# Kernel tuning notes

Hardware: AMD Instinct MI355X
Metric: run time of the kernel (lower is better)

The kernel has to match this reference:

```python
import jax, jax.numpy as jnp
import numpy as np

MIN_K = 1024  # hard-negative mining floor per image (per_image=True branch)


def setup_inputs() -> dict:
    key = jax.random.key(0)
    k1, k2 = jax.random.split(key)
    B, C, D, H, W = 4, 3, 64, 256, 256
    inp = jax.random.normal(k1, (B, C, D, H, W), dtype=jnp.float32)
    tgt = jax.random.randint(k2, (B, D, H, W), 0, C, dtype=jnp.int64)
    return {"input": inp, "target": tgt}


def reference(input, target):
    b = input.shape[0]
    # per-pixel cross-entropy: -log_softmax over class dim, gathered at target
    logp = jax.nn.log_softmax(input, axis=1)                      # [B,C,D,H,W]
    ce = -jnp.take_along_axis(logp, target[:, None].astype(jnp.int32), axis=1)[:, 0]
    loss = ce.reshape(b, -1)                                      # [B, N]
    tflat = target.reshape(b, -1)                                 # [B, N]
    N = loss.shape[1]

    fg = tflat > 0                                                # [B, N]
    fg_num = fg.sum(axis=1)                                       # [B] int
    bg_num = N - fg_num                                           # [B] int
    k = jnp.minimum(bg_num, jnp.maximum(fg_num, MIN_K))           # [B] int

    # foreground term: mean of fg losses (0 if no fg)
    fg_sum = jnp.where(fg, loss, 0.0).sum(axis=1)                 # [B]
    fg_term = jnp.where(fg_num > 0,
                        fg_sum / jnp.maximum(fg_num, 1).astype(loss.dtype), 0.0)

    # background term: mean of top-k hardest bg losses (data-dependent k, fixed shapes)
    bg_masked = jnp.where(fg, -jnp.inf, loss)                     # fg -> -inf, never selected
    sorted_desc = -jnp.sort(-bg_masked, axis=1)                   # [B, N] descending
    sel = jnp.arange(N)[None, :] < k[:, None]                     # first k entries
    bg_sum = jnp.where(sel, sorted_desc, 0.0).sum(axis=1)         # [B]
    bg_term = jnp.where(bg_num > 0,
                        bg_sum / jnp.maximum(k, 1).astype(loss.dtype), 0.0)

    return jnp.sum(fg_term + bg_term) / b
```

## Files before the change

### kernel.cpp

```cpp
#include <hip/hip_runtime.h>

#define NPIX 4194304
#define BATCH 4
#define MINK 1024ULL
#define NBINS 4096
#define G1 1024
#define HG 256

typedef unsigned long long u64;
typedef int vint4 __attribute__((ext_vector_type(4)));

__device__ __forceinline__ float pix_loss(float v0, float v1, float v2, int t) {
    float m = fmaxf(fmaxf(v0, v1), v2);
    float lse = m + __logf(__expf(v0 - m) + __expf(v1 - m) + __expf(v2 - m));
    float xt = (t == 0) ? v0 : ((t == 1) ? v1 : v2);
    return lse - xt;
}

__global__ __launch_bounds__(256) void k_reduce(const float* __restrict__ x,
                                                const int* __restrict__ tg,
                                                float* __restrict__ pfs,
                                                float* __restrict__ pbs,
                                                unsigned* __restrict__ pfc) {
    const int b = blockIdx.y;
    const float* xb = x + (size_t)b * 3 * NPIX;
    const int* tb = tg + (size_t)b * NPIX;
    float fs = 0.f, bs = 0.f;
    int fc = 0;
    const int stride = G1 * 256 * 4;
#pragma unroll
    for (int it = 0; it < NPIX / stride; ++it) {
        const int i = it * stride + (blockIdx.x * 256 + threadIdx.x) * 4;
        const float4 a = *(const float4*)(xb + i);
        const float4 c = *(const float4*)(xb + NPIX + i);
        const float4 d = *(const float4*)(xb + 2 * NPIX + i);
        const vint4 t4 = __builtin_nontemporal_load((const vint4*)(tb + i));
        float l;
        l = pix_loss(a.x, c.x, d.x, t4[0]); if (t4[0] > 0) { fs += l; fc++; } else bs += l;
        l = pix_loss(a.y, c.y, d.y, t4[1]); if (t4[1] > 0) { fs += l; fc++; } else bs += l;
        l = pix_loss(a.z, c.z, d.z, t4[2]); if (t4[2] > 0) { fs += l; fc++; } else bs += l;
        l = pix_loss(a.w, c.w, d.w, t4[3]); if (t4[3] > 0) { fs += l; fc++; } else bs += l;
    }
#pragma unroll
    for (int off = 32; off > 0; off >>= 1) {
        fs += __shfl_down(fs, off);
        bs += __shfl_down(bs, off);
        fc += __shfl_down(fc, off);
    }
    __shared__ float sfs[4], sbs[4];
    __shared__ int sfc[4];
    const int wid = threadIdx.x >> 6;
    if ((threadIdx.x & 63) == 0) { sfs[wid] = fs; sbs[wid] = bs; sfc[wid] = fc; }
    __syncthreads();
    if (threadIdx.x == 0) {
        const int slot = b * G1 + blockIdx.x;
        pfs[slot] = sfs[0] + sfs[1] + sfs[2] + sfs[3];
        pbs[slot] = sbs[0] + sbs[1] + sbs[2] + sbs[3];
        pfc[slot] = (unsigned)(sfc[0] + sfc[1] + sfc[2] + sfc[3]);
    }
}

__global__ __launch_bounds__(256) void k_sumfin(const float* __restrict__ pfs,
                                                const float* __restrict__ pbs,
                                                const unsigned* __restrict__ pfc,
                                                double* __restrict__ fg_sum,
                                                double* __restrict__ bg_sum,
                                                u64* __restrict__ fg_cnt,
                                                unsigned* __restrict__ hist_cnt,
                                                float* __restrict__ hist_sum,
                                                unsigned* __restrict__ flags,
                                                float* __restrict__ out,
                                                int have_hist) {
    __shared__ double sd0[4], sd1[4];
    __shared__ u64 sc[4];
    __shared__ double tfs[BATCH], tbs[BATCH];
    __shared__ u64 tfc[BATCH];
    const float4* pfs4 = (const float4*)pfs;
    const float4* pbs4 = (const float4*)pbs;
    const uint4* pfc4 = (const uint4*)pfc;
    for (int b = 0; b < BATCH; ++b) {
        const float4 f4 = pfs4[b * (G1 / 4) + threadIdx.x];
        const float4 b4 = pbs4[b * (G1 / 4) + threadIdx.x];
        const uint4 c4 = pfc4[b * (G1 / 4) + threadIdx.x];
        double fs = (double)f4.x + (double)f4.y + (double)f4.z + (double)f4.w;
        double bs = (double)b4.x + (double)b4.y + (double)b4.z + (double)b4.w;
        u64 fc = (u64)c4.x + c4.y + c4.z + c4.w;
#pragma unroll
        for (int off = 32; off > 0; off >>= 1) {
            fs += __shfl_down(fs, off);
            bs += __shfl_down(bs, off);
            fc += __shfl_down(fc, off);
        }
        const int wid = threadIdx.x >> 6;
        if ((threadIdx.x & 63) == 0) { sd0[wid] = fs; sd1[wid] = bs; sc[wid] = fc; }
        __syncthreads();
        if (threadIdx.x == 0) {
            tfs[b] = sd0[0] + sd0[1] + sd0[2] + sd0[3];
            tbs[b] = sd1[0] + sd1[1] + sd1[2] + sd1[3];
            tfc[b] = sc[0] + sc[1] + sc[2] + sc[3];
            fg_sum[b] = tfs[b];
            bg_sum[b] = tbs[b];
            fg_cnt[b] = tfc[b];
        }
        __syncthreads();
    }
    if (threadIdx.x == 0) {
        double acc = 0.0;
        unsigned need = 0u;
        for (int b = 0; b < BATCH; ++b) {
            const u64 fc = tfc[b];
            const u64 bg = (u64)NPIX - fc;
            u64 mk = fc > MINK ? fc : MINK;
            const u64 k = bg < mk ? bg : mk;
            double fg_term = (fc > 0) ? tfs[b] / (double)fc : 0.0;
            u64 kd = k > 1 ? k : 1;
            double bg_term = (bg > 0) ? tbs[b] / (double)kd : 0.0;
            if (k < bg && have_hist) need |= (1u << b);
            acc += fg_term + bg_term;
        }
        out[0] = (float)(acc / (double)BATCH);
        flags[0] = need;
        flags[1] = 0u;
    }
    if (have_hist) {
        uint4 z4 = make_uint4(0u, 0u, 0u, 0u);
        uint4* hc4 = (uint4*)hist_cnt;
        uint4* hs4 = (uint4*)hist_sum;
        for (int i = threadIdx.x; i < BATCH * NBINS / 4; i += 256) {
            hc4[i] = z4;
            hs4[i] = z4;
        }
    }
}

__global__ __launch_bounds__(256) void k_hist(const float* __restrict__ x,
                                              const int* __restrict__ tg,
                                              const double* __restrict__ fg_sum,
                                              const double* __restrict__ bg_sum,
                                              const u64* __restrict__ fg_cnt,
                                              unsigned* __restrict__ hist_cnt,
                                              float* __restrict__ hist_sum,
                                              unsigned* __restrict__ flags,
                                              float* __restrict__ out) {
    const unsigned need = flags[0];
    if (need == 0u) return;

    const int b = blockIdx.y;
    __shared__ unsigned hc[NBINS];
    __shared__ float hs[NBINS];

    if (need & (1u << b)) {
        for (int i = threadIdx.x; i < NBINS; i += 256) { hc[i] = 0u; hs[i] = 0.f; }
        __syncthreads();
        const float* xb = x + (size_t)b * 3 * NPIX;
        const int* tb = tg + (size_t)b * NPIX;
        const int stride = HG * 256 * 4;
        for (int i = (blockIdx.x * 256 + threadIdx.x) * 4; i < NPIX; i += stride) {
            const float4 a = *(const float4*)(xb + i);
            const float4 c = *(const float4*)(xb + NPIX + i);
            const float4 d = *(const float4*)(xb + 2 * NPIX + i);
            const int4 t4 = *(const int4*)(tb + i);
            float v[4][3] = {{a.x, c.x, d.x}, {a.y, c.y, d.y}, {a.z, c.z, d.z}, {a.w, c.w, d.w}};
            int tt[4] = {t4.x, t4.y, t4.z, t4.w};
#pragma unroll
            for (int j = 0; j < 4; ++j) {
                if (tt[j] == 0) {
                    float l = fmaxf(pix_loss(v[j][0], v[j][1], v[j][2], tt[j]), 0.f);
                    unsigned bin = __float_as_uint(l) >> 20;
                    atomicAdd(&hc[bin], 1u);
                    atomicAdd(&hs[bin], l);
                }
            }
        }
        __syncthreads();
        for (int i = threadIdx.x; i < NBINS; i += 256) {
            if (hc[i]) {
                atomicAdd(&hist_cnt[(size_t)b * NBINS + i], hc[i]);
                atomicAdd(&hist_sum[(size_t)b * NBINS + i], hs[i]);
            }
        }
    }

    __threadfence();
    __syncthreads();
    __shared__ int is_last;
    if (threadIdx.x == 0) {
        unsigned v = atomicAdd(&flags[1], 1u);
        is_last = (v == (unsigned)(HG * BATCH) - 1u) ? 1 : 0;
    }
    __syncthreads();
    if (!is_last) return;

    __threadfence();
    __shared__ double sbt[BATCH];
    for (int b2 = 0; b2 < BATCH; ++b2) {
        if (need & (1u << b2)) {
            for (int i = threadIdx.x; i < NBINS; i += 256) {
                hc[i] = __hip_atomic_load(&hist_cnt[(size_t)b2 * NBINS + i],
                                          __ATOMIC_ACQUIRE, __HIP_MEMORY_SCOPE_AGENT);
                hs[i] = __hip_atomic_load(&hist_sum[(size_t)b2 * NBINS + i],
                                          __ATOMIC_ACQUIRE, __HIP_MEMORY_SCOPE_AGENT);
            }
            __syncthreads();
            if (threadIdx.x == 0) {
                const u64 fc = fg_cnt[b2];
                const u64 bg = (u64)NPIX - fc;
                u64 mk = fc > MINK ? fc : MINK;
                const u64 k = bg < mk ? bg : mk;
                u64 cnt = 0;
                double s = 0.0, bg_topk = 0.0;
                for (int i = NBINS - 1; i >= 0; --i) {
                    unsigned c = hc[i];
                    if (cnt + c >= k) {
                        double edge = (double)__uint_as_float(((unsigned)i) << 20);
                        bg_topk = s + (double)(k - cnt) * edge;
                        break;
                    }
                    cnt += c;
                    s += (double)hs[i];
                }
                sbt[b2] = bg_topk;
            }
            __syncthreads();
        }
    }
    if (threadIdx.x == 0) {
        double acc = 0.0;
        for (int b2 = 0; b2 < BATCH; ++b2) {
            const u64 fc = fg_cnt[b2];
            const u64 bg = (u64)NPIX - fc;
            u64 mk = fc > MINK ? fc : MINK;
            const u64 k = bg < mk ? bg : mk;
            double fg_term = (fc > 0) ? fg_sum[b2] / (double)fc : 0.0;
            double bg_topk = (need & (1u << b2)) ? sbt[b2] : bg_sum[b2];
            u64 kd = k > 1 ? k : 1;
            double bg_term = (bg > 0) ? bg_topk / (double)kd : 0.0;
            acc += fg_term + bg_term;
        }
        out[0] = (float)(acc / (double)BATCH);
    }
}

extern "C" void kernel_launch(void* const* d_in, const int* in_sizes, int n_in,
                              void* d_out, int out_size, void* d_ws, size_t ws_size,
                              hipStream_t stream) {
    const float* x = (const float*)d_in[0];
    const int* tg = (const int*)d_in[1];
    float* out = (float*)d_out;

    char* ws = (char*)d_ws;
    float* pfs = (float*)ws;
    float* pbs = (float*)(ws + 16384);
    unsigned* pfc = (unsigned*)(ws + 32768);
    double* fg_sum = (double*)(ws + 49152);
    double* bg_sum = (double*)(ws + 49184);
    u64* fg_cnt = (u64*)(ws + 49216);
    unsigned* flags = (unsigned*)(ws + 49248);
    unsigned* hist_cnt = (unsigned*)(ws + 49280);
    float* hist_sum = (float*)(ws + 49280 + (size_t)BATCH * NBINS * 4);
    const size_t need_ws = 49280 + (size_t)BATCH * NBINS * 8;
    const int have_hist = (ws_size >= need_ws) ? 1 : 0;

    dim3 block(256);
    dim3 grid1(G1, BATCH);
    k_reduce<<<grid1, block, 0, stream>>>(x, tg, pfs, pbs, pfc);
    k_sumfin<<<1, block, 0, stream>>>(pfs, pbs, pfc, fg_sum, bg_sum, fg_cnt,
                                      hist_cnt, hist_sum, flags, out, have_hist);
    if (have_hist) {
        dim3 hgrid(HG, BATCH);
        k_hist<<<hgrid, block, 0, stream>>>(x, tg, fg_sum, bg_sum, fg_cnt,
                                            hist_cnt, hist_sum, flags, out);
    }
}
```

Baseline: 55.29 us.

## Fuse finalize and histogram kernels into one tail kernel, zero histogram in reduce

After: 52.13 us. 1.06x faster.

```diff
diff --git a/kernel.cpp b/kernel.cpp
--- a/kernel.cpp
+++ b/kernel.cpp
@@ -21,8 +21,15 @@
                                                 const int* __restrict__ tg,
                                                 float* __restrict__ pfs,
                                                 float* __restrict__ pbs,
-                                                unsigned* __restrict__ pfc) {
+                                                unsigned* __restrict__ pfc,
+                                                uint4* __restrict__ histz,
+                                                unsigned* __restrict__ flags,
+                                                int have_hist) {
     const int b = blockIdx.y;
+    if (b == 0 && blockIdx.x < 32) {
+        if (have_hist) histz[blockIdx.x * 256 + threadIdx.x] = make_uint4(0u, 0u, 0u, 0u);
+        if (blockIdx.x == 0 && threadIdx.x == 0) flags[1] = 0u;
+    }
     const float* xb = x + (size_t)b * 3 * NPIX;
     const int* tb = tg + (size_t)b * NPIX;
     float fs = 0.f, bs = 0.f;
@@ -60,102 +67,95 @@
     }
 }
 
-__global__ __launch_bounds__(256) void k_sumfin(const float* __restrict__ pfs,
-                                                const float* __restrict__ pbs,
-                                                const unsigned* __restrict__ pfc,
-                                                double* __restrict__ fg_sum,
-                                                double* __restrict__ bg_sum,
-                                                u64* __restrict__ fg_cnt,
-                                                unsigned* __restrict__ hist_cnt,
-                                                float* __restrict__ hist_sum,
-                                                unsigned* __restrict__ flags,
-                                                float* __restrict__ out,
-                                                int have_hist) {
-    __shared__ double sd0[4], sd1[4];
-    __shared__ u64 sc[4];
-    __shared__ double tfs[BATCH], tbs[BATCH];
-    __shared__ u64 tfc[BATCH];
-    const float4* pfs4 = (const float4*)pfs;
-    const float4* pbs4 = (const float4*)pbs;
-    const uint4* pfc4 = (const uint4*)pfc;
-    for (int b = 0; b < BATCH; ++b) {
-        const float4 f4 = pfs4[b * (G1 / 4) + threadIdx.x];
-        const float4 b4 = pbs4[b * (G1 / 4) + threadIdx.x];
-        const uint4 c4 = pfc4[b * (G1 / 4) + threadIdx.x];
-        double fs = (double)f4.x + (double)f4.y + (double)f4.z + (double)f4.w;
-        double bs = (double)b4.x + (double)b4.y + (double)b4.z + (double)b4.w;
-        u64 fc = (u64)c4.x + c4.y + c4.z + c4.w;
-#pragma unroll
-        for (int off = 32; off > 0; off >>= 1) {
-            fs += __shfl_down(fs, off);
-            bs += __shfl_down(bs, off);
-            fc += __shfl_down(fc, off);
-        }
-        const int wid = threadIdx.x >> 6;
-        if ((threadIdx.x & 63) == 0) { sd0[wid] = fs; sd1[wid] = bs; sc[wid] = fc; }
-        __syncthreads();
-        if (threadIdx.x == 0) {
-            tfs[b] = sd0[0] + sd0[1] + sd0[2] + sd0[3];
-            tbs[b] = sd1[0] + sd1[1] + sd1[2] + sd1[3];
-            tfc[b] = sc[0] + sc[1] + sc[2] + sc[3];
-            fg_sum[b] = tfs[b];
-            bg_sum[b] = tbs[b];
-            fg_cnt[b] = tfc[b];
-        }
-        __syncthreads();
-    }
-    if (threadIdx.x == 0) {
-        double acc = 0.0;
-        unsigned need = 0u;
-        for (int b = 0; b < BATCH; ++b) {
-            const u64 fc = tfc[b];
-            const u64 bg = (u64)NPIX - fc;
-            u64 mk = fc > MINK ? fc : MINK;
-            const u64 k = bg < mk ? bg : mk;
-            double fg_term = (fc > 0) ? tfs[b] / (double)fc : 0.0;
-            u64 kd = k > 1 ? k : 1;
-            double bg_term = (bg > 0) ? tbs[b] / (double)kd : 0.0;
-            if (k < bg && have_hist) need |= (1u << b);
-            acc += fg_term + bg_term;
-        }
-        out[0] = (float)(acc / (double)BATCH);
-        flags[0] = need;
-        flags[1] = 0u;
-    }
-    if (have_hist) {
-        uint4 z4 = make_uint4(0u, 0u, 0u, 0u);
-        uint4* hc4 = (uint4*)hist_cnt;
-        uint4* hs4 = (uint4*)hist_sum;
-        for (int i = threadIdx.x; i < BATCH * NBINS / 4; i += 256) {
-            hc4[i] = z4;
-            hs4[i] = z4;
-        }
-    }
-}
-
-__global__ __launch_bounds__(256) void k_hist(const float* __restrict__ x,
+__device__ __forceinline__ void reduce_image(const float* __restrict__ pfs,
+                                             const float* __restrict__ pbs,
+                                             const unsigned* __restrict__ pfc,
+                                             int b2, int tid,
+                                             double* __restrict__ sda,
+                                             double* __restrict__ sdb,
+                                             unsigned* __restrict__ su,
+                                             double& tfs, double& tbs, u64& tfc) {
+    const float4 f4 = ((const float4*)pfs)[b2 * (G1 / 4) + tid];
+    const float4 b4 = ((const float4*)pbs)[b2 * (G1 / 4) + tid];
+    const uint4 c4 = ((const uint4*)pfc)[b2 * (G1 / 4) + tid];
+    double fs = (double)f4.x + (double)f4.y + (double)f4.z + (double)f4.w;
+    double bs = (double)b4.x + (double)b4.y + (double)b4.z + (double)b4.w;
+    unsigned fc = c4.x + c4.y + c4.z + c4.w;
+#pragma unroll
+    for (int off = 32; off > 0; off >>= 1) {
+        fs += __shfl_down(fs, off);
+        bs += __shfl_down(bs, off);
+        fc += __shfl_down(fc, off);
+    }
+    const int wid = tid >> 6;
+    if ((tid & 63) == 0) { sda[wid] = fs; sdb[wid] = bs; su[wid] = fc; }
+    __syncthreads();
+    tfs = sda[0] + sda[1] + sda[2] + sda[3];
+    tbs = sdb[0] + sdb[1] + sdb[2] + sdb[3];
+    tfc = (u64)su[0] + su[1] + su[2] + su[3];
+    __syncthreads();
+}
+
+__global__ __launch_bounds__(256) void k_tail(const float* __restrict__ pfs,
+                                              const float* __restrict__ pbs,
+                                              const unsigned* __restrict__ pfc,
+                                              const float* __restrict__ x,
                                               const int* __restrict__ tg,
-                                              const double* __restrict__ fg_sum,
-                                              const double* __restrict__ bg_sum,
-                                              const u64* __restrict__ fg_cnt,
                                               unsigned* __restrict__ hist_cnt,
                                               float* __restrict__ hist_sum,
                                               unsigned* __restrict__ flags,
-                                              float* __restrict__ out) {
-    const unsigned need = flags[0];
-    if (need == 0u) return;
-
+                                              float* __restrict__ out,
+                                              int have_hist) {
     const int b = blockIdx.y;
+    const int tid = threadIdx.x;
+    __shared__ double sda[4], sdb[4];
+    __shared__ unsigned su[4];
+
+    u64 fc_own;
+    {
+        const uint4 c4 = ((const uint4*)pfc)[b * (G1 / 4) + tid];
+        unsigned s = c4.x + c4.y + c4.z + c4.w;
+#pragma unroll
+        for (int off = 32; off > 0; off >>= 1) s += __shfl_down(s, off);
+        if ((tid & 63) == 0) su[tid >> 6] = s;
+        __syncthreads();
+        fc_own = (u64)su[0] + su[1] + su[2] + su[3];
+        __syncthreads();
+    }
+    const u64 bg_own = (u64)NPIX - fc_own;
+    const u64 mk_own = fc_own > MINK ? fc_own : MINK;
+    const u64 k_own = bg_own < mk_own ? bg_own : mk_own;
+    const bool need_own = (k_own < bg_own) && have_hist;
+
+    if (blockIdx.x == 0 && b == 0) {
+        double acc = 0.0;
+        bool any_need = false;
+        for (int b2 = 0; b2 < BATCH; ++b2) {
+            double tfs, tbs; u64 tfc;
+            reduce_image(pfs, pbs, pfc, b2, tid, sda, sdb, su, tfs, tbs, tfc);
+            const u64 bg = (u64)NPIX - tfc;
+            const u64 mk = tfc > MINK ? tfc : MINK;
+            const u64 k = bg < mk ? bg : mk;
+            if (k < bg && have_hist) any_need = true;
+            const double fg_term = (tfc > 0) ? tfs / (double)tfc : 0.0;
+            const u64 kd = k > 1 ? k : 1;
+            const double bg_term = (bg > 0) ? tbs / (double)kd : 0.0;
+            acc += fg_term + bg_term;
+        }
+        if (tid == 0 && !any_need) out[0] = (float)(acc / (double)BATCH);
+    }
+
+    if (!need_own) return;
+
     __shared__ unsigned hc[NBINS];
     __shared__ float hs[NBINS];
-
-    if (need & (1u << b)) {
-        for (int i = threadIdx.x; i < NBINS; i += 256) { hc[i] = 0u; hs[i] = 0.f; }
-        __syncthreads();
+    for (int i = tid; i < NBINS; i += 256) { hc[i] = 0u; hs[i] = 0.f; }
+    __syncthreads();
+    {
         const float* xb = x + (size_t)b * 3 * NPIX;
         const int* tb = tg + (size_t)b * NPIX;
         const int stride = HG * 256 * 4;
-        for (int i = (blockIdx.x * 256 + threadIdx.x) * 4; i < NPIX; i += stride) {
+        for (int i = (blockIdx.x * 256 + tid) * 4; i < NPIX; i += stride) {
             const float4 a = *(const float4*)(xb + i);
             const float4 c = *(const float4*)(xb + NPIX + i);
             const float4 d = *(const float4*)(xb + 2 * NPIX + i);
@@ -172,73 +172,82 @@
                 }
             }
         }
-        __syncthreads();
-        for (int i = threadIdx.x; i < NBINS; i += 256) {
-            if (hc[i]) {
-                atomicAdd(&hist_cnt[(size_t)b * NBINS + i], hc[i]);
-                atomicAdd(&hist_sum[(size_t)b * NBINS + i], hs[i]);
-            }
-        }
+    }
+    __syncthreads();
+    for (int i = tid; i < NBINS; i += 256) {
+        if (hc[i]) {
+            atomicAdd(&hist_cnt[(size_t)b * NBINS + i], hc[i]);
+            atomicAdd(&hist_sum[(size_t)b * NBINS + i], hs[i]);
+        }
+    }
+
+    int nneed = 0;
+    for (int b2 = 0; b2 < BATCH; ++b2) {
+        const uint4 c4 = ((const uint4*)pfc)[b2 * (G1 / 4) + tid];
+        unsigned s = c4.x + c4.y + c4.z + c4.w;
+#pragma unroll
+        for (int off = 32; off > 0; off >>= 1) s += __shfl_down(s, off);
+        if ((tid & 63) == 0) su[tid >> 6] = s;
+        __syncthreads();
+        const u64 fc2 = (u64)su[0] + su[1] + su[2] + su[3];
+        __syncthreads();
+        const u64 bg2 = (u64)NPIX - fc2;
+        const u64 mk2 = fc2 > MINK ? fc2 : MINK;
+        const u64 k2 = bg2 < mk2 ? bg2 : mk2;
+        if (k2 < bg2) nneed++;
     }
 
     __threadfence();
     __syncthreads();
     __shared__ int is_last;
-    if (threadIdx.x == 0) {
+    if (tid == 0) {
         unsigned v = atomicAdd(&flags[1], 1u);
-        is_last = (v == (unsigned)(HG * BATCH) - 1u) ? 1 : 0;
+        is_last = (v == (unsigned)(HG * nneed) - 1u) ? 1 : 0;
     }
     __syncthreads();
     if (!is_last) return;
-
     __threadfence();
-    __shared__ double sbt[BATCH];
+
+    double acc = 0.0;
     for (int b2 = 0; b2 < BATCH; ++b2) {
-        if (need & (1u << b2)) {
-            for (int i = threadIdx.x; i < NBINS; i += 256) {
+        double tfs, tbs; u64 tfc;
+        reduce_image(pfs, pbs, pfc, b2, tid, sda, sdb, su, tfs, tbs, tfc);
+        const u64 bg = (u64)NPIX - tfc;
+        const u64 mk = tfc > MINK ? tfc : MINK;
+        const u64 k = bg < mk ? bg : mk;
+        double bg_sel = tbs;
+        if (k < bg) {
+            for (int i = tid; i < NBINS; i += 256) {
                 hc[i] = __hip_atomic_load(&hist_cnt[(size_t)b2 * NBINS + i],
                                           __ATOMIC_ACQUIRE, __HIP_MEMORY_SCOPE_AGENT);
                 hs[i] = __hip_atomic_load(&hist_sum[(size_t)b2 * NBINS + i],
                                           __ATOMIC_ACQUIRE, __HIP_MEMORY_SCOPE_AGENT);
             }
             __syncthreads();
-            if (threadIdx.x == 0) {
-                const u64 fc = fg_cnt[b2];
-                const u64 bg = (u64)NPIX - fc;
-                u64 mk = fc > MINK ? fc : MINK;
-                const u64 k = bg < mk ? bg : mk;
-                u64 cnt = 0;
-                double s = 0.0, bg_topk = 0.0;
+            if (tid == 0) {
+                u64 cnt = 0; double s = 0.0, topk = 0.0;
                 for (int i = NBINS - 1; i >= 0; --i) {
                     unsigned c = hc[i];
                     if (cnt + c >= k) {
                         double edge = (double)__uint_as_float(((unsigned)i) << 20);
-                        bg_topk = s + (double)(k - cnt) * edge;
+                        topk = s + (double)(k - cnt) * edge;
                         break;
                     }
                     cnt += c;
                     s += (double)hs[i];
                 }
-                sbt[b2] = bg_topk;
+                sda[0] = topk;
             }
             __syncthreads();
-        }
-    }
-    if (threadIdx.x == 0) {
-        double acc = 0.0;
-        for (int b2 = 0; b2 < BATCH; ++b2) {
-            const u64 fc = fg_cnt[b2];
-            const u64 bg = (u64)NPIX - fc;
-            u64 mk = fc > MINK ? fc : MINK;
-            const u64 k = bg < mk ? bg : mk;
-            double fg_term = (fc > 0) ? fg_sum[b2] / (double)fc : 0.0;
-            double bg_topk = (need & (1u << b2)) ? sbt[b2] : bg_sum[b2];
-            u64 kd = k > 1 ? k : 1;
-            double bg_term = (bg > 0) ? bg_topk / (double)kd : 0.0;
-            acc += fg_term + bg_term;
-        }
-        out[0] = (float)(acc / (double)BATCH);
-    }
+            bg_sel = sda[0];
+            __syncthreads();
+        }
+        const double fg_term = (tfc > 0) ? tfs / (double)tfc : 0.0;
+        const u64 kd = k > 1 ? k : 1;
+        const double bg_term = (bg > 0) ? bg_sel / (double)kd : 0.0;
+        acc += fg_term + bg_term;
+    }
+    if (tid == 0) out[0] = (float)(acc / (double)BATCH);
 }
 
 extern "C" void kernel_launch(void* const* d_in, const int* in_sizes, int n_in,
@@ -252,23 +261,17 @@
     float* pfs = (float*)ws;
     float* pbs = (float*)(ws + 16384);
     unsigned* pfc = (unsigned*)(ws + 32768);
-    double* fg_sum = (double*)(ws + 49152);
-    double* bg_sum = (double*)(ws + 49184);
-    u64* fg_cnt = (u64*)(ws + 49216);
-    unsigned* flags = (unsigned*)(ws + 49248);
+    unsigned* flags = (unsigned*)(ws + 49152);
     unsigned* hist_cnt = (unsigned*)(ws + 49280);
     float* hist_sum = (float*)(ws + 49280 + (size_t)BATCH * NBINS * 4);
+    uint4* histz = (uint4*)(ws + 49280);
     const size_t need_ws = 49280 + (size_t)BATCH * NBINS * 8;
     const int have_hist = (ws_size >= need_ws) ? 1 : 0;
 
     dim3 block(256);
     dim3 grid1(G1, BATCH);
-    k_reduce<<<grid1, block, 0, stream>>>(x, tg, pfs, pbs, pfc);
-    k_sumfin<<<1, block, 0, stream>>>(pfs, pbs, pfc, fg_sum, bg_sum, fg_cnt,
-                                      hist_cnt, hist_sum, flags, out, have_hist);
-    if (have_hist) {
-        dim3 hgrid(HG, BATCH);
-        k_hist<<<hgrid, block, 0, stream>>>(x, tg, fg_sum, bg_sum, fg_cnt,
-                                            hist_cnt, hist_sum, flags, out);
-    }
-}
+    k_reduce<<<grid1, block, 0, stream>>>(x, tg, pfs, pbs, pfc, histz, flags, have_hist);
+    dim3 grid2(HG, BATCH);
+    k_tail<<<grid2, block, 0, stream>>>(pfs, pbs, pfc, x, tg,
+                                        hist_cnt, hist_sum, flags, out, have_hist);
+}
```
